# Optimization experiments

Measured on AMD Instinct MI355X. Metric: run time of the kernel, lower is better.

Reference implementation:

```python
import jax, jax.numpy as jnp
import numpy as np

BN_EPS = 1e-5


def _gcn(x, A, W, gamma, beta):
    # x: [B,N,Cin], A: [B,N,N] -> [B,N,Cout]; BatchNorm1d over (B,N) per channel (train-mode batch stats)
    h = jnp.einsum('bnm,bmc->bnc', A, x @ W)
    mu = h.mean(axis=(0, 1))
    var = h.var(axis=(0, 1))
    h = (h - mu) * jax.lax.rsqrt(var + BN_EPS) * gamma + beta
    return jax.nn.relu(h)  # dropout is identity (drop_prob=0 / eval)


def _ppige(x, A, W0, g0, b0, W_res, g_res, b_res):
    h = _gcn(x, A, W0, g0, b0)
    for i in range(W_res.shape[0]):  # residual GCN stack (num_GCN-1 layers)
        h = _gcn(h, A, W_res[i], g_res[i], b_res[i]) + h
    return h


def _gge(x, w1, b1, w2, b2):
    return jax.nn.relu(jax.nn.relu(x @ w1 + b1) @ w2 + b2)


def _gaga(G, h):
    # G: [B,N,H], h: [B,H]
    att = jax.nn.softmax(jnp.einsum('bnh,bh->bn', G, h), axis=-1)
    return jnp.einsum('bnh,bn->bh', G, att)


def _led(ea, eb, conv_w, conv_b, p1_w, p1_b, p2_w, p2_b):
    # ea, eb: [B, 2H]; Conv1d(2H->2H, k=1) over length-2 axis then MaxPool1d(2)
    stacked = jnp.stack([ea, eb], axis=-1)  # [B, 2H, 2]
    conv = jnp.einsum('oc,bct->bot', conv_w, stacked) + conv_b[None, :, None]
    cnn_x = conv.max(axis=-1)  # [B, 2H]
    x = jax.nn.relu(jnp.concatenate([cnn_x, ea - eb], axis=1) @ p1_w + p1_b)
    return x @ p2_w + p2_b


def setup_inputs() -> dict:
    key = jax.random.key(0)
    ks = jax.random.split(key, 24)
    Bs, N, PPI_in, H, F_in = 8, 2048, 512, 256, 1024
    n_res = 3  # num_GCN - 1
    s = 0.02
    adjA = jax.random.uniform(ks[0], (Bs, N, N), jnp.float32)
    adjB = jax.random.uniform(ks[1], (Bs, N, N), jnp.float32)
    adjA = adjA / adjA.sum(-1, keepdims=True)  # row-normalized for numerical sanity
    adjB = adjB / adjB.sum(-1, keepdims=True)
    return {
        'a': jax.random.normal(ks[2], (Bs, F_in), jnp.float32),
        'bio_a': jax.random.normal(ks[3], (Bs, N, PPI_in), jnp.float32),
        'A': adjA,
        'b': jax.random.normal(ks[4], (Bs, F_in), jnp.float32),
        'bio_b': jax.random.normal(ks[5], (Bs, N, PPI_in), jnp.float32),
        'B': adjB,
        'W0': jax.random.normal(ks[6], (PPI_in, H), jnp.float32) * s,
        'gamma0': jnp.ones((H,), jnp.float32),
        'beta0': jnp.zeros((H,), jnp.float32),
        'W_res': jax.random.normal(ks[7], (n_res, H, H), jnp.float32) * s,
        'gamma_res': jnp.ones((n_res, H), jnp.float32),
        'beta_res': jnp.zeros((n_res, H), jnp.float32),
        'g1_w': jax.random.normal(ks[8], (F_in, 128), jnp.float32) * s,
        'g1_b': jnp.zeros((128,), jnp.float32),
        'g2_w': jax.random.normal(ks[9], (128, H), jnp.float32) * s,
        'g2_b': jnp.zeros((H,), jnp.float32),
        'conv_w': jax.random.normal(ks[10], (2 * H, 2 * H), jnp.float32) * s,
        'conv_b': jnp.zeros((2 * H,), jnp.float32),
        'p1_w': jax.random.normal(ks[11], (4 * H, H), jnp.float32) * s,
        'p1_b': jnp.zeros((H,), jnp.float32),
        'p2_w': jax.random.normal(ks[12], (H, 2), jnp.float32) * s,
        'p2_b': jnp.zeros((2,), jnp.float32),
    }


def reference(a, bio_a, A, b, bio_b, B, W0, gamma0, beta0, W_res, gamma_res, beta_res,
              g1_w, g1_b, g2_w, g2_b, conv_w, conv_b, p1_w, p1_b, p2_w, p2_b):
    Ga = _ppige(bio_a, A, W0, gamma0, beta0, W_res, gamma_res, beta_res)
    Gb = _ppige(bio_b, B, W0, gamma0, beta0, W_res, gamma_res, beta_res)
    ha = _gge(a, g1_w, g1_b, g2_w, g2_b)
    hb = _gge(b, g1_w, g1_b, g2_w, g2_b)
    ea = jnp.concatenate([ha, _gaga(Ga, ha)], axis=-1)
    eb = jnp.concatenate([hb, _gaga(Gb, hb)], axis=-1)
    logits = _led(ea, eb, conv_w, conv_b, p1_w, p1_b, p2_w, p2_b)
    return jax.nn.log_softmax(logits, axis=-1)
```

## Files before the change

kernel.cpp:

```cpp
#include <hip/hip_runtime.h>
#include <hip/hip_bf16.h>
#include <cstdint>

typedef unsigned short u16;
typedef __bf16 bf16x8 __attribute__((ext_vector_type(8)));
typedef float f32x4 __attribute__((ext_vector_type(4)));

typedef __attribute__((address_space(1))) const void* gas_ptr;
typedef __attribute__((address_space(3))) void* las_ptr;

__device__ __forceinline__ u16 f2bf(float f) {
  union { __hip_bfloat16 h; u16 u; } v;
  v.h = __float2bfloat16(f);
  return v.u;
}
__device__ __forceinline__ float bf2f(u16 u) {
  union { unsigned int i; float f; } v;
  v.i = ((unsigned int)u) << 16;
  return v.f;
}

__device__ __forceinline__ void gload16(const u16* g, u16* l) {
  __builtin_amdgcn_global_load_lds((gas_ptr)g, (las_ptr)l, 16, 0, 0);
}

__global__ __launch_bounds__(256) void k_prep_weights(const float* __restrict__ W0,
                                                      const float* __restrict__ Wres,
                                                      u16* __restrict__ W0t,
                                                      u16* __restrict__ Wrt) {
  __shared__ float tile[32][33];
  int y = blockIdx.y;
  const float* src; u16* dst; int R, r0;
  if (y < 16) { src = W0; dst = W0t; R = 512; r0 = y * 32; }
  else {
    int i = (y - 16) >> 3;
    src = Wres + i * 65536; dst = Wrt + i * 65536; R = 256; r0 = ((y - 16) & 7) * 32;
  }
  const int C = 256;
  int c0 = blockIdx.x * 32;
  int tx = threadIdx.x & 31, ty = threadIdx.x >> 5;
#pragma unroll
  for (int i = 0; i < 4; ++i) {
    int r = ty + i * 8;
    tile[r][tx] = src[(long)(r0 + r) * C + c0 + tx];
  }
  __syncthreads();
#pragma unroll
  for (int i = 0; i < 4; ++i) {
    int c = ty + i * 8;
    dst[(long)(c0 + c) * R + r0 + tx] = f2bf(tile[tx][c]);
  }
}

template<int EPI, int SWZ, int CVT>
__global__ __launch_bounds__(256) void k_gemm(
    const u16* __restrict__ A, int lda, long sA,
    const float* __restrict__ Afa, const float* __restrict__ Afb,
    long splitRow, int ldaf, long zrows, u16* __restrict__ AbfOut,
    const u16* __restrict__ Bt, int ldb, long sB,
    u16* __restrict__ C, int ldc, long sC,
    u16* __restrict__ PtOut, int ldpt,
    float* __restrict__ stats, int K) {
  __shared__ __align__(16) u16 smem[4][8192];
  __shared__ float cs[256];
  const int tid = threadIdx.x;
  const int lane = tid & 63;
  const int wid = tid >> 6;
  const int wm = wid >> 1, wn = wid & 1;

  int bx = blockIdx.x, by = blockIdx.y, bz = blockIdx.z;
  if (SWZ == 1) {
    int lin = bx + 16 * by + 32 * bz;
    int swz = (lin & 7) * 64 + (lin >> 3);
    bx = swz & 15; by = (swz >> 4) & 1; bz = swz >> 5;
  } else if (SWZ == 2) {
    int t = bx; bx = by; by = t;
  }
  const long m0 = (long)bx * 128, n0 = (long)by * 128;
  const int z = bz;
  const u16* Ab = A + (long)z * sA;
  const u16* Btb = Bt + (long)z * sB;

  const int rsub = lane >> 3;
  const int swzcol = ((lane & 7) ^ rsub) * 8;
  const long a_row = m0 + wid * 32 + rsub;
  const long b_row = n0 + wid * 32 + rsub;

  if (EPI == 0) cs[tid] = 0.f;

  const f32x4 zero = {0.f, 0.f, 0.f, 0.f};
  f32x4 acc[4][4];
#pragma unroll
  for (int i = 0; i < 4; ++i)
#pragma unroll
    for (int j = 0; j < 4; ++j) acc[i][j] = zero;

  const int fr = lane & 15;
  const int kgrp = lane >> 4;
  const int swz_rd = lane & 7;
  const int nk = K >> 6;

  auto stageA = [&](int buf, int k0) {
#pragma unroll
    for (int i = 0; i < 4; ++i)
      gload16(Ab + (a_row + i * 8) * lda + (k0 + swzcol), &smem[buf][(wid * 32 + i * 8) * 64]);
  };
  auto stageB = [&](int buf, int k0) {
#pragma unroll
    for (int i = 0; i < 4; ++i)
      gload16(Btb + (b_row + i * 8) * ldb + (k0 + swzcol), &smem[2 + buf][(wid * 32 + i * 8) * 64]);
  };
  auto compute = [&](const u16* Asb, const u16* Bsb) {
#pragma unroll
    for (int ks = 0; ks < 2; ++ks) {
      bf16x8 af[4], bfv[4];
#pragma unroll
      for (int f = 0; f < 4; ++f) {
        int cA = (ks * 4 + kgrp) ^ swz_rd;
        af[f]  = *reinterpret_cast<const bf16x8*>(&Asb[(wm * 64 + f * 16 + fr) * 64 + cA * 8]);
        bfv[f] = *reinterpret_cast<const bf16x8*>(&Bsb[(wn * 64 + f * 16 + fr) * 64 + cA * 8]);
      }
#pragma unroll
      for (int mf = 0; mf < 4; ++mf)
#pragma unroll
        for (int nf = 0; nf < 4; ++nf)
          acc[mf][nf] = __builtin_amdgcn_mfma_f32_16x16x32_bf16(af[mf], bfv[nf], acc[mf][nf], 0, 0, 0);
    }
  };

#define RLOADA(k0)                                                                       \
  {                                                                                      \
    _Pragma("unroll")                                                                    \
    for (int i = 0; i < 4; ++i) {                                                        \
      long R = (long)z * zrows + a_row + i * 8;                                          \
      const float* sp = (R < splitRow ? Afa + R * (long)ldaf                             \
                                      : Afb + (R - splitRow) * (long)ldaf) + (k0) + swzcol; \
      rg[i * 2]     = *reinterpret_cast<const float4*>(sp);                              \
      rg[i * 2 + 1] = *reinterpret_cast<const float4*>(sp + 4);                          \
    }                                                                                    \
  }
#define CVTWRITEA(buf, k0)                                                               \
  {                                                                                      \
    _Pragma("unroll")                                                                    \
    for (int i = 0; i < 4; ++i) {                                                        \
      union { u16 u[8]; uint4 q; } o;                                                    \
      o.u[0] = f2bf(rg[i*2].x);   o.u[1] = f2bf(rg[i*2].y);                              \
      o.u[2] = f2bf(rg[i*2].z);   o.u[3] = f2bf(rg[i*2].w);                              \
      o.u[4] = f2bf(rg[i*2+1].x); o.u[5] = f2bf(rg[i*2+1].y);                            \
      o.u[6] = f2bf(rg[i*2+1].z); o.u[7] = f2bf(rg[i*2+1].w);                            \
      *reinterpret_cast<uint4*>(&smem[buf][(wid * 32 + i * 8) * 64 + lane * 8]) = o.q;   \
      if (AbfOut && by == 0) {                                                           \
        long R = (long)z * zrows + a_row + i * 8;                                        \
        *reinterpret_cast<uint4*>(AbfOut + R * (long)ldaf + (k0) + swzcol) = o.q;        \
      }                                                                                  \
    }                                                                                    \
  }

  if constexpr (CVT) {
    float4 rg[8];
    RLOADA(0);
    stageB(0, 0);
    CVTWRITEA(0, 0);
    __syncthreads();
    for (int t = 0; t < nk; ++t) {
      int cur = t & 1;
      if (t + 1 < nk) { RLOADA((t + 1) * 64); stageB(1 - cur, (t + 1) * 64); }
      compute(smem[cur], smem[2 + cur]);
      if (t + 1 < nk) CVTWRITEA(1 - cur, (t + 1) * 64);
      __syncthreads();
    }
  } else {
    stageA(0, 0); stageB(0, 0);
    __syncthreads();
    for (int t = 0; t < nk; ++t) {
      int cur = t & 1;
      if (t + 1 < nk) { stageA(1 - cur, (t + 1) * 64); stageB(1 - cur, (t + 1) * 64); }
      compute(smem[cur], smem[2 + cur]);
      __syncthreads();
    }
  }
#undef RLOADA
#undef CVTWRITEA

  if (EPI == 0) {
    u16* Cb = C + (long)z * sC;
    const int side = z >> 3;
#pragma unroll
    for (int mf = 0; mf < 4; ++mf) {
      long mrow = m0 + wm * 64 + mf * 16 + kgrp * 4;
#pragma unroll
      for (int nf = 0; nf < 4; ++nf) {
        long ncol = n0 + wn * 64 + nf * 16 + fr;
#pragma unroll
        for (int r = 0; r < 4; ++r)
          Cb[(mrow + r) * ldc + ncol] = f2bf(acc[mf][nf][r]);
      }
    }
#pragma unroll
    for (int nf = 0; nf < 4; ++nf) {
      int cl = wn * 64 + nf * 16 + fr;
      float s = 0.f, q = 0.f;
#pragma unroll
      for (int mf = 0; mf < 4; ++mf)
#pragma unroll
        for (int r = 0; r < 4; ++r) { float v = acc[mf][nf][r]; s += v; q += v * v; }
      atomicAdd(&cs[cl], s);
      atomicAdd(&cs[128 + cl], q);
    }
    __syncthreads();
    if (tid < 128) atomicAdd(&stats[side * 512 + n0 + tid], cs[tid]);
    else           atomicAdd(&stats[side * 512 + 256 + n0 + (tid - 128)], cs[tid]);
  } else {
    u16* Ts = &smem[0][0];
#pragma unroll
    for (int mf = 0; mf < 4; ++mf)
#pragma unroll
      for (int nf = 0; nf < 4; ++nf) {
        int nl = wn * 64 + nf * 16 + fr;
        int ml = wm * 64 + mf * 16 + kgrp * 4;
#pragma unroll
        for (int r = 0; r < 4; ++r)
          Ts[nl * 136 + ml + r] = f2bf(acc[mf][nf][r]);
      }
    __syncthreads();
    int n = tid >> 1, half = tid & 1;
    const u16* sp = Ts + n * 136 + half * 64;
    u16* dp = PtOut + (long)(n0 + n) * ldpt + m0 + half * 64;
#pragma unroll
    for (int j = 0; j < 8; ++j)
      reinterpret_cast<uint4*>(dp)[j] = reinterpret_cast<const uint4*>(sp)[j];
  }
}

__global__ __launch_bounds__(256) void k_bn_apply(const ushort4* __restrict__ u4,
                                                  ushort4* __restrict__ h4,
                                                  const float* __restrict__ statsL,
                                                  const float* __restrict__ gamma,
                                                  const float* __restrict__ beta, int res) {
  long i = (long)blockIdx.x * 256 + threadIdx.x;
  int side = (int)(i >> 20);
  int c0 = (int)(i & 63) * 4;
  const float* st = statsL + side * 512;
  ushort4 uv = u4[i];
  float vp[4] = { bf2f(uv.x), bf2f(uv.y), bf2f(uv.z), bf2f(uv.w) };
  float rp[4];
#pragma unroll
  for (int j = 0; j < 4; ++j) {
    int c = c0 + j;
    float mu = st[c] * (1.f / 16384.f);
    float var = st[256 + c] * (1.f / 16384.f) - mu * mu;
    float sc = gamma[c] * rsqrtf(var + 1e-5f);
    float sh = beta[c] - mu * sc;
    rp[j] = fmaxf(vp[j] * sc + sh, 0.f);
  }
  if (res) {
    ushort4 hv = h4[i];
    rp[0] += bf2f(hv.x); rp[1] += bf2f(hv.y); rp[2] += bf2f(hv.z); rp[3] += bf2f(hv.w);
  }
  ushort4 o;
  o.x = f2bf(rp[0]); o.y = f2bf(rp[1]); o.z = f2bf(rp[2]); o.w = f2bf(rp[3]);
  h4[i] = o;
}

__global__ __launch_bounds__(256) void k_gge(const float* __restrict__ in_a,
                                             const float* __restrict__ in_b,
                                             const float* __restrict__ w1, const float* __restrict__ b1,
                                             const float* __restrict__ w2, const float* __restrict__ b2,
                                             float* __restrict__ ha) {
  __shared__ float av[1024];
  __shared__ float hid[128];
  int bx = blockIdx.x, t = threadIdx.x;
  const float* ap = ((bx >> 3) ? in_b : in_a) + (bx & 7) * 1024;
  for (int i = t; i < 1024; i += 256) av[i] = ap[i];
  __syncthreads();
  if (t < 128) {
    float s = b1[t];
    for (int c = 0; c < 1024; ++c) s += av[c] * w1[c * 128 + t];
    hid[t] = fmaxf(s, 0.f);
  }
  __syncthreads();
  float s = b2[t];
  for (int c = 0; c < 128; ++c) s += hid[c] * w2[c * 256 + t];
  ha[bx * 256 + t] = fmaxf(s, 0.f);
}

__global__ __launch_bounds__(256) void k_gaga_scores(const u16* __restrict__ h,
                                                     const float* __restrict__ ha,
                                                     float* __restrict__ sc) {
  __shared__ __align__(16) float has[256];
  int bx = blockIdx.x;
  has[threadIdx.x] = ha[bx * 256 + threadIdx.x];
  __syncthreads();
  const u16* G = h + (long)bx * 524288;
  int wv = threadIdx.x >> 6, lane = threadIdx.x & 63;
  float4 h4 = reinterpret_cast<const float4*>(has)[lane];
  for (int i = 0; i < 32; ++i) {
    int n = blockIdx.y * 128 + wv * 32 + i;
    ushort4 v = reinterpret_cast<const ushort4*>(G + (long)n * 256)[lane];
    float d = bf2f(v.x) * h4.x + bf2f(v.y) * h4.y + bf2f(v.z) * h4.z + bf2f(v.w) * h4.w;
#pragma unroll
    for (int o2 = 32; o2 > 0; o2 >>= 1) d += __shfl_down(d, o2);
    if (lane == 0) sc[bx * 2048 + n] = d;
  }
}

__global__ __launch_bounds__(256) void k_softmax2048(const float* __restrict__ sc, float* __restrict__ att) {
  __shared__ float red[256];
  int b = blockIdx.x, t = threadIdx.x;
  const float* s = sc + b * 2048;
  float* o = att + b * 2048;
  float v[8];
  float m = -1e30f;
#pragma unroll
  for (int i = 0; i < 8; ++i) { v[i] = s[t + i * 256]; m = fmaxf(m, v[i]); }
  red[t] = m; __syncthreads();
  for (int o2 = 128; o2 > 0; o2 >>= 1) { if (t < o2) red[t] = fmaxf(red[t], red[t + o2]); __syncthreads(); }
  m = red[0]; __syncthreads();
  float sum = 0.f;
#pragma unroll
  for (int i = 0; i < 8; ++i) { v[i] = expf(v[i] - m); sum += v[i]; }
  red[t] = sum; __syncthreads();
  for (int o2 = 128; o2 > 0; o2 >>= 1) { if (t < o2) red[t] += red[t + o2]; __syncthreads(); }
  float inv = 1.f / red[0];
#pragma unroll
  for (int i = 0; i < 8; ++i) o[t + i * 256] = v[i] * inv;
}

__global__ __launch_bounds__(256) void k_gaga_out(const u16* __restrict__ h,
                                                  const float* __restrict__ att,
                                                  float* __restrict__ ga) {
  __shared__ float atts[128];
  int bx = blockIdx.x, n0 = blockIdx.y * 128, c = threadIdx.x;
  if (threadIdx.x < 128) atts[threadIdx.x] = att[bx * 2048 + n0 + threadIdx.x];
  __syncthreads();
  const u16* base = h + (long)bx * 524288 + (long)n0 * 256 + c;
  float s = 0.f;
#pragma unroll 4
  for (int i = 0; i < 128; ++i) s += bf2f(base[(long)i * 256]) * atts[i];
  atomicAdd(&ga[bx * 256 + c], s);
}

__global__ __launch_bounds__(512) void k_led_conv(const float* __restrict__ ha, const float* __restrict__ ga,
                                                  const float* __restrict__ hb, const float* __restrict__ gb,
                                                  const float* __restrict__ cw, const float* __restrict__ cb,
                                                  float* __restrict__ cnn, float* __restrict__ diff) {
  __shared__ float ea[8][512], eb[8][512];
  int t = threadIdx.x;
  for (int i = t; i < 4096; i += 512) {
    int b = i >> 9, c = i & 511;
    float va = (c < 256) ? ha[b * 256 + c] : ga[b * 256 + c - 256];
    float vb = (c < 256) ? hb[b * 256 + c] : gb[b * 256 + c - 256];
    ea[b][c] = va; eb[b][c] = vb;
    if (blockIdx.x == 0) diff[i] = va - vb;
  }
  __syncthreads();
  int o = blockIdx.x * 64 + (t >> 3), b = t & 7;
  const float* wr = cw + (long)o * 512;
  float s0 = cb[o], s1 = s0;
  for (int c = 0; c < 512; ++c) { float w = wr[c]; s0 += w * ea[b][c]; s1 += w * eb[b][c]; }
  cnn[b * 512 + o] = fmaxf(s0, s1);
}

__global__ __launch_bounds__(256) void k_led_p1(const float* __restrict__ cnn, const float* __restrict__ diff,
                                                const float* __restrict__ w, const float* __restrict__ pb,
                                                float* __restrict__ x) {
  __shared__ float cat[8][1024];
  int t = threadIdx.x;
  for (int i = t; i < 8192; i += 256) {
    int b = i >> 10, c = i & 1023;
    cat[b][c] = (c < 512) ? cnn[b * 512 + c] : diff[b * 512 + c - 512];
  }
  __syncthreads();
  int o = blockIdx.x * 32 + (t >> 3), b = t & 7;
  float s = pb[o];
  for (int c = 0; c < 1024; ++c) s += cat[b][c] * w[c * 256 + o];
  x[b * 256 + o] = fmaxf(s, 0.f);
}

__global__ __launch_bounds__(64) void k_led_final(const float* __restrict__ x,
                                                  const float* __restrict__ p2w, const float* __restrict__ p2b,
                                                  float* __restrict__ out) {
  __shared__ float lg[16];
  int t = threadIdx.x;
  if (t < 16) {
    int b = t >> 1, j = t & 1;
    float s = p2b[j];
    for (int c = 0; c < 256; ++c) s += x[b * 256 + c] * p2w[c * 2 + j];
    lg[t] = s;
  }
  __syncthreads();
  if (t < 8) {
    float l0 = lg[t * 2], l1 = lg[t * 2 + 1];
    float m = fmaxf(l0, l1);
    float lse = m + logf(expf(l0 - m) + expf(l1 - m));
    out[t * 2] = l0 - lse;
    out[t * 2 + 1] = l1 - lse;
  }
}

extern "C" void kernel_launch(void* const* d_in, const int* in_sizes, int n_in,
                              void* d_out, int out_size, void* d_ws, size_t ws_size,
                              hipStream_t stream) {
  const float* in_a   = (const float*)d_in[0];
  const float* bio_a  = (const float*)d_in[1];
  const float* adj_a  = (const float*)d_in[2];
  const float* in_b   = (const float*)d_in[3];
  const float* bio_b  = (const float*)d_in[4];
  const float* adj_b  = (const float*)d_in[5];
  const float* W0     = (const float*)d_in[6];
  const float* gamma0 = (const float*)d_in[7];
  const float* beta0  = (const float*)d_in[8];
  const float* W_res  = (const float*)d_in[9];
  const float* g_res  = (const float*)d_in[10];
  const float* b_res  = (const float*)d_in[11];
  const float* g1_w   = (const float*)d_in[12];
  const float* g1_b   = (const float*)d_in[13];
  const float* g2_w   = (const float*)d_in[14];
  const float* g2_b   = (const float*)d_in[15];
  const float* conv_w = (const float*)d_in[16];
  const float* conv_b = (const float*)d_in[17];
  const float* p1_w   = (const float*)d_in[18];
  const float* p1_b   = (const float*)d_in[19];
  const float* p2_w   = (const float*)d_in[20];
  const float* p2_b   = (const float*)d_in[21];
  float* out = (float*)d_out;

  char* ws = (char*)d_ws;
  size_t off = 0;
  auto alloc = [&](size_t bytes) {
    char* p = ws + off;
    off += (bytes + 255) & ~(size_t)255;
    return p;
  };
  u16*   Abf   = (u16*)  alloc(67108864ull * 2);
  u16*   Pt    = (u16*)  alloc(8388608ull * 2);
  u16*   ubf   = (u16*)  alloc(8388608ull * 2);
  u16*   hbf   = (u16*)  alloc(8388608ull * 2);
  u16*   W0t   = (u16*)  alloc(131072ull * 2);
  u16*   Wrt   = (u16*)  alloc(196608ull * 2);
  float* stats = (float*)alloc(4096 * 4);
  float* gabuf = (float*)alloc(4096 * 4);
  float* hav   = (float*)alloc(4096 * 4);
  float* scb   = (float*)alloc(32768 * 4);
  float* attb  = (float*)alloc(32768 * 4);
  float* cnn   = (float*)alloc(4096 * 4);
  float* diff  = (float*)alloc(4096 * 4);
  float* xbuf  = (float*)alloc(2048 * 4);

  k_prep_weights<<<dim3(8, 40), 256, 0, stream>>>(W0, W_res, W0t, Wrt);
  (void)hipMemsetAsync(stats, 0, 32768, stream);

  for (int layer = 0; layer < 4; ++layer) {
    float* statsL = stats + layer * 1024;
    const float* gm = (layer == 0) ? gamma0 : (g_res + (layer - 1) * 256);
    const float* bt = (layer == 0) ? beta0 : (b_res + (layer - 1) * 256);

    if (layer == 0) {
      k_gemm<1, 2, 1><<<dim3(2, 256, 1), 256, 0, stream>>>(
          nullptr, 0, 0, bio_a, bio_b, 16384L, 512, 0, nullptr,
          W0t, 512, 0, nullptr, 0, 0, Pt, 32768, nullptr, 512);
      k_gemm<0, 1, 1><<<dim3(16, 2, 16), 256, 0, stream>>>(
          nullptr, 0, 0, adj_a, adj_b, 16384L, 2048, 2048, Abf,
          Pt, 32768, 2048, ubf, 256, 524288L, nullptr, 0, statsL, 2048);
    } else {
      const u16* Wt = Wrt + (layer - 1) * 65536;
      k_gemm<1, 2, 0><<<dim3(2, 256, 1), 256, 0, stream>>>(
          hbf, 256, 0, nullptr, nullptr, 0, 0, 0, nullptr,
          Wt, 256, 0, nullptr, 0, 0, Pt, 32768, nullptr, 256);
      k_gemm<0, 1, 0><<<dim3(16, 2, 16), 256, 0, stream>>>(
          Abf, 2048, 4194304L, nullptr, nullptr, 0, 0, 0, nullptr,
          Pt, 32768, 2048, ubf, 256, 524288L, nullptr, 0, statsL, 2048);
    }
    k_bn_apply<<<8192, 256, 0, stream>>>((const ushort4*)ubf, (ushort4*)hbf,
                                         statsL, gm, bt, layer ? 1 : 0);
  }

  k_gge<<<16, 256, 0, stream>>>(in_a, in_b, g1_w, g1_b, g2_w, g2_b, hav);
  k_gaga_scores<<<dim3(16, 16), 256, 0, stream>>>(hbf, hav, scb);
  k_softmax2048<<<16, 256, 0, stream>>>(scb, attb);
  k_gaga_out<<<dim3(16, 16), 256, 0, stream>>>(hbf, attb, gabuf);

  k_led_conv<<<8, 512, 0, stream>>>(hav, gabuf, hav + 2048, gabuf + 2048, conv_w, conv_b, cnn, diff);
  k_led_p1<<<8, 256, 0, stream>>>(cnn, diff, p1_w, p1_b, xbuf);
  k_led_final<<<1, 64, 0, stream>>>(xbuf, p2_w, p2_b, out);
}
```

Measured before the change: 557.1 us.

## Single-buffer A tile via registers to cut LDS and raise occupancy

The GEMM kernel drops from double-buffered A and B tiles in LDS to a single A buffer plus double-buffered B, which shrinks shared memory from 64KB to 48KB. A is now always loaded through registers and written to LDS after a barrier. The bf16 path also switches from direct global-to-LDS loads to this register path, and launch bounds request 3 blocks per CU. The aim is higher occupancy to hide latency. In exchange there is an extra barrier per k-step, the A write is serialized after compute, and register pressure rises under the tighter bound, which may cause spills.

```diff
diff --git a/kernel.cpp b/kernel.cpp
--- a/kernel.cpp
+++ b/kernel.cpp
@@ -53,7 +53,7 @@
 }
 
 template<int EPI, int SWZ, int CVT>
-__global__ __launch_bounds__(256) void k_gemm(
+__global__ __launch_bounds__(256, 3) void k_gemm(
     const u16* __restrict__ A, int lda, long sA,
     const float* __restrict__ Afa, const float* __restrict__ Afb,
     long splitRow, int ldaf, long zrows, u16* __restrict__ AbfOut,
@@ -61,7 +61,7 @@
     u16* __restrict__ C, int ldc, long sC,
     u16* __restrict__ PtOut, int ldpt,
     float* __restrict__ stats, int K) {
-  __shared__ __align__(16) u16 smem[4][8192];
+  __shared__ __align__(16) u16 smem[24576];
   __shared__ float cs[256];
   const int tid = threadIdx.x;
   const int lane = tid & 63;
@@ -100,15 +100,51 @@
   const int swz_rd = lane & 7;
   const int nk = K >> 6;
 
-  auto stageA = [&](int buf, int k0) {
+  float4 rgf[8];
+  uint4 rgu[4];
+
+  auto stageB = [&](int bufofs, int k0) {
 #pragma unroll
     for (int i = 0; i < 4; ++i)
-      gload16(Ab + (a_row + i * 8) * lda + (k0 + swzcol), &smem[buf][(wid * 32 + i * 8) * 64]);
+      gload16(Btb + (b_row + i * 8) * (long)ldb + (k0 + swzcol),
+              &smem[bufofs + (wid * 32 + i * 8) * 64]);
   };
-  auto stageB = [&](int buf, int k0) {
-#pragma unroll
-    for (int i = 0; i < 4; ++i)
-      gload16(Btb + (b_row + i * 8) * ldb + (k0 + swzcol), &smem[2 + buf][(wid * 32 + i * 8) * 64]);
+  auto loadA = [&](int k0) {
+    if constexpr (CVT) {
+#pragma unroll
+      for (int i = 0; i < 4; ++i) {
+        long R = (long)z * zrows + a_row + i * 8;
+        const float* sp = (R < splitRow ? Afa + R * (long)ldaf
+                                        : Afb + (R - splitRow) * (long)ldaf) + k0 + swzcol;
+        rgf[i * 2] = *reinterpret_cast<const float4*>(sp);
+        rgf[i * 2 + 1] = *reinterpret_cast<const float4*>(sp + 4);
+      }
+    } else {
+#pragma unroll
+      for (int i = 0; i < 4; ++i)
+        rgu[i] = *reinterpret_cast<const uint4*>(Ab + (a_row + i * 8) * (long)lda + k0 + swzcol);
+    }
+  };
+  auto writeA = [&](int k0) {
+#pragma unroll
+    for (int i = 0; i < 4; ++i) {
+      uint4 q;
+      if constexpr (CVT) {
+        union { u16 u[8]; uint4 qq; } o;
+        o.u[0] = f2bf(rgf[i*2].x);   o.u[1] = f2bf(rgf[i*2].y);
+        o.u[2] = f2bf(rgf[i*2].z);   o.u[3] = f2bf(rgf[i*2].w);
+        o.u[4] = f2bf(rgf[i*2+1].x); o.u[5] = f2bf(rgf[i*2+1].y);
+        o.u[6] = f2bf(rgf[i*2+1].z); o.u[7] = f2bf(rgf[i*2+1].w);
+        q = o.qq;
+        if (AbfOut && by == 0) {
+          long R = (long)z * zrows + a_row + i * 8;
+          *reinterpret_cast<uint4*>(AbfOut + R * (long)ldaf + k0 + swzcol) = q;
+        }
+      } else {
+        q = rgu[i];
+      }
+      *reinterpret_cast<uint4*>(&smem[(wid * 32 + i * 8) * 64 + lane * 8]) = q;
+    }
   };
   auto compute = [&](const u16* Asb, const u16* Bsb) {
 #pragma unroll
@@ -128,59 +164,21 @@
     }
   };
 
-#define RLOADA(k0)                                                                       \
-  {                                                                                      \
-    _Pragma("unroll")                                                                    \
-    for (int i = 0; i < 4; ++i) {                                                        \
-      long R = (long)z * zrows + a_row + i * 8;                                          \
-      const float* sp = (R < splitRow ? Afa + R * (long)ldaf                             \
-                                      : Afb + (R - splitRow) * (long)ldaf) + (k0) + swzcol; \
-      rg[i * 2]     = *reinterpret_cast<const float4*>(sp);                              \
-      rg[i * 2 + 1] = *reinterpret_cast<const float4*>(sp + 4);                          \
-    }                                                                                    \
-  }
-#define CVTWRITEA(buf, k0)                                                               \
-  {                                                                                      \
-    _Pragma("unroll")                                                                    \
-    for (int i = 0; i < 4; ++i) {                                                        \
-      union { u16 u[8]; uint4 q; } o;                                                    \
-      o.u[0] = f2bf(rg[i*2].x);   o.u[1] = f2bf(rg[i*2].y);                              \
-      o.u[2] = f2bf(rg[i*2].z);   o.u[3] = f2bf(rg[i*2].w);                              \
-      o.u[4] = f2bf(rg[i*2+1].x); o.u[5] = f2bf(rg[i*2+1].y);                            \
-      o.u[6] = f2bf(rg[i*2+1].z); o.u[7] = f2bf(rg[i*2+1].w);                            \
-      *reinterpret_cast<uint4*>(&smem[buf][(wid * 32 + i * 8) * 64 + lane * 8]) = o.q;   \
-      if (AbfOut && by == 0) {                                                           \
-        long R = (long)z * zrows + a_row + i * 8;                                        \
-        *reinterpret_cast<uint4*>(AbfOut + R * (long)ldaf + (k0) + swzcol) = o.q;        \
-      }                                                                                  \
-    }                                                                                    \
-  }
-
-  if constexpr (CVT) {
-    float4 rg[8];
-    RLOADA(0);
-    stageB(0, 0);
-    CVTWRITEA(0, 0);
+  stageB(8192, 0);
+  loadA(0);
+  writeA(0);
+  __syncthreads();
+  for (int t = 0; t < nk; ++t) {
+    const u16* Bsb = &smem[8192 + ((t & 1) << 13)];
+    if (t + 1 < nk) {
+      stageB(8192 + ((~t & 1) << 13), (t + 1) * 64);
+      loadA((t + 1) * 64);
+    }
+    compute(smem, Bsb);
     __syncthreads();
-    for (int t = 0; t < nk; ++t) {
-      int cur = t & 1;
-      if (t + 1 < nk) { RLOADA((t + 1) * 64); stageB(1 - cur, (t + 1) * 64); }
-      compute(smem[cur], smem[2 + cur]);
-      if (t + 1 < nk) CVTWRITEA(1 - cur, (t + 1) * 64);
-      __syncthreads();
-    }
-  } else {
-    stageA(0, 0); stageB(0, 0);
+    if (t + 1 < nk) writeA((t + 1) * 64);
     __syncthreads();
-    for (int t = 0; t < nk; ++t) {
-      int cur = t & 1;
-      if (t + 1 < nk) { stageA(1 - cur, (t + 1) * 64); stageB(1 - cur, (t + 1) * 64); }
-      compute(smem[cur], smem[2 + cur]);
-      __syncthreads();
-    }
-  }
-#undef RLOADA
-#undef CVTWRITEA
+  }
 
   if (EPI == 0) {
     u16* Cb = C + (long)z * sC;
@@ -211,7 +209,7 @@
     if (tid < 128) atomicAdd(&stats[side * 512 + n0 + tid], cs[tid]);
     else           atomicAdd(&stats[side * 512 + 256 + n0 + (tid - 128)], cs[tid]);
   } else {
-    u16* Ts = &smem[0][0];
+    u16* Ts = &smem[0];
 #pragma unroll
     for (int mf = 0; mf < 4; ++mf)
 #pragma unroll
```

Measured after the change: 563.9 us. No clear change (+1.2%).
